# Kernel optimization log

Hardware: AMD Instinct MI355X
Metric: run time of the kernel (lower is better)

The kernel has to match this reference:

```python
import jax, jax.numpy as jnp
import numpy as np

N = 100000   # nodes
E = 1600000  # edges (avg degree 16)
H = 128      # hidden_channels
OUT = 64     # out_channels


def setup_inputs() -> dict:
    key = jax.random.key(0)
    ks = jax.random.split(key, 12)
    def lin(k, fan_in, fan_out):
        s = 1.0 / np.sqrt(fan_in)
        kw, kb = jax.random.split(k)
        W = jax.random.uniform(kw, (fan_in, fan_out), jnp.float32, -s, s)
        b = jax.random.uniform(kb, (fan_out,), jnp.float32, -s, s)
        return W, b
    W1, b1 = lin(ks[2], 1, H)
    W2, b2 = lin(ks[3], H, H)
    W3, b3 = lin(ks[4], H, H)
    Wo, bo = lin(ks[5], H, OUT)
    return {
        "x": jax.random.normal(ks[0], (N, 1), jnp.float32),
        "edge_index": jax.random.randint(ks[1], (2, E), 0, N, jnp.int32),
        "W1": W1, "b1": b1,
        "W2": W2, "b2": b2,
        "W3": W3, "b3": b3,
        "Wo": Wo, "bo": bo,
    }


def _gcn_conv(x, W, b, src, dst, dinv):
    # PyG GCNConv: x' = W x, then deg-normalized scatter-add over edges (+bias)
    h = x @ W                              # [N, C_out]
    norm = dinv[src] * dinv[dst]           # [E+N]
    msg = h[src] * norm[:, None]           # gather + scale  [E+N, C_out]
    out = jax.ops.segment_sum(msg, dst, num_segments=N)  # scatter-add
    return out + b


def reference(x, edge_index, W1, b1, W2, b2, W3, b3, Wo, bo):
    # add self-loops (GCNConv default add_self_loops=True)
    loop = jnp.arange(N, dtype=edge_index.dtype)
    src = jnp.concatenate([edge_index[0], loop])
    dst = jnp.concatenate([edge_index[1], loop])
    # symmetric normalization: deg over destination nodes, weight=1
    deg = jax.ops.segment_sum(jnp.ones_like(dst, jnp.float32), dst, num_segments=N)
    dinv = jnp.where(deg > 0, jax.lax.rsqrt(jnp.maximum(deg, 1.0)), 0.0)

    # layer 1: GCNConv -> dropout(eval=identity) -> relu
    h = jax.nn.relu(_gcn_conv(x, W1, b1, src, dst, dinv))
    # mid layer (num_layers=3 -> one mid block): GCNConv -> dropout -> relu
    h = jax.nn.relu(_gcn_conv(h, W2, b2, src, dst, dinv))
    # last layer: GCNConv -> dropout (no relu)
    h = _gcn_conv(h, W3, b3, src, dst, dinv)
    # linear head
    return h @ Wo + bo
```

## Files before the change

### kernel.cpp

```cpp
#include <hip/hip_runtime.h>

#define GN 100000
#define GE 1600000
#define GH 128
#define GOUT 64

#define NBUCK 391
#define BK 256
#define BCAP 4608
#define P1B 196
#define P1E 8192

#define NPW 5
#define CAPE 110
#define CAPW 112

typedef _Float16 half8v __attribute__((ext_vector_type(8)));
typedef _Float16 half4v __attribute__((ext_vector_type(4)));
typedef _Float16 half2v __attribute__((ext_vector_type(2)));
typedef float floatx4 __attribute__((ext_vector_type(4)));

__device__ __forceinline__ float dot2acc(half2v a, half2v b, float c) {
#if __has_builtin(__builtin_amdgcn_fdot2)
  return __builtin_amdgcn_fdot2(a, b, c, false);
#else
  return fmaf((float)a[0], (float)b[0], fmaf((float)a[1], (float)b[1], c));
#endif
}


__global__ __launch_bounds__(512) void k_zero(int* __restrict__ gCnt) {
  gCnt[threadIdx.x] = 0;
}


__global__ __launch_bounds__(1024) void p1_prep(const int* __restrict__ ei, int* __restrict__ gCnt,
                                                unsigned* __restrict__ staged,
                                                const float* __restrict__ W1, const float* __restrict__ b1,
                                                const float* __restrict__ W2, const float* __restrict__ W3,
                                                const float* __restrict__ Wo, const float* __restrict__ b3,
                                                const float* __restrict__ bo, unsigned* __restrict__ tabS,
                                                float* __restrict__ knots, _Float16* __restrict__ Wch,
                                                float* __restrict__ bch, int* __restrict__ rowStart) {
  int tid = threadIdx.x;
  int blk = blockIdx.x;
  if (blk < P1B) {
    __shared__ int cur[NBUCK];
    __shared__ int base[NBUCK];
    if (tid < NBUCK) cur[tid] = 0;
    __syncthreads();
    int e0 = blk * P1E;
    int sv[8], dv[8];
#pragma unroll
    for (int k = 0; k < 8; ++k) {
      int e = e0 + k * 1024 + tid;
      if (e < GE) {
        sv[k] = ei[e];
        dv[k] = ei[GE + e];
      } else {
        sv[k] = 0;
        dv[k] = -1;
      }
    }
#pragma unroll
    for (int k = 0; k < 8; ++k) {
      if (dv[k] >= 0) atomicAdd(&cur[dv[k] >> 8], 1);
    }
    __syncthreads();
    if (tid < NBUCK) {
      base[tid] = atomicAdd(&gCnt[tid], cur[tid]);
      cur[tid] = 0;
    }
    __syncthreads();
#pragma unroll
    for (int k = 0; k < 8; ++k) {
      if (dv[k] >= 0) {
        int bb = dv[k] >> 8;
        int r = atomicAdd(&cur[bb], 1);
        int pos = base[bb] + r;
        if (pos < BCAP) staged[(size_t)bb * BCAP + pos] = ((unsigned)sv[k] << 8) | (unsigned)(dv[k] & 255);
      }
    }
  } else if (blk == P1B) {
    __shared__ _Float16 sW2[GH * GH];
    __shared__ float sW1[GH], sb1[GH], th[GH];
    __shared__ int sidx[GH];
    for (int i = tid; i < GH * GH / 4; i += 1024) {
      float4 v = ((const float4*)W2)[i];
      half4v h;
      h[0] = (_Float16)v.x; h[1] = (_Float16)v.y; h[2] = (_Float16)v.z; h[3] = (_Float16)v.w;
      ((half4v*)sW2)[i] = h;
    }
    if (tid < GH) {
      float w1 = W1[tid], bb = b1[tid];
      sW1[tid] = w1;
      sb1[tid] = bb;
      th[tid] = (w1 != 0.0f) ? (-bb / w1) : 3.0e38f;
    }
    __syncthreads();
    if (tid < GH) {
      float my = th[tid];
      int r = 0;
      for (int j = 0; j < GH; ++j) {
        float tj = th[j];
        r += (tj < my) || (tj == my && j < tid);
      }
      sidx[r] = tid;
      knots[r] = my;
    }
    __syncthreads();
    if (tid < GH) {
      int c = tid;
      float A = 0.f, B = 0.f;
      for (int k = 0; k < GH; ++k) {
        float w1 = sW1[k];
        float w2 = (float)sW2[k * GH + c];
        if (w1 < 0.0f) {
          A = fmaf(w1, w2, A);
          B = fmaf(sb1[k], w2, B);
        } else if (w1 == 0.0f && sb1[k] > 0.0f) {
          B = fmaf(sb1[k], w2, B);
        }
      }
      for (int b = 0; b <= GH; ++b) {
        half2v hh;
        hh[0] = (_Float16)A;
        hh[1] = (_Float16)B;
        tabS[((b * 64 + (c >> 1)) << 1) + (c & 1)] = __builtin_bit_cast(unsigned, hh);
        if (b < GH) {
          int k = sidx[b];
          float w1 = sW1[k];
          float w2 = (float)sW2[k * GH + c];
          if (w1 > 0.0f) {
            A = fmaf(w1, w2, A);
            B = fmaf(sb1[k], w2, B);
          } else if (w1 < 0.0f) {
            A = fmaf(-w1, w2, A);
            B = fmaf(-sb1[k], w2, B);
          }
        }
      }
    }
  } else if (blk <= P1B + 8) {
    int idx = (blk - P1B - 1) * 1024 + tid;
    int k = idx >> 6, c = idx & 63;
    float s = 0.f;
#pragma unroll 8
    for (int j = 0; j < GH; ++j) s = fmaf(W3[k * GH + j], Wo[j * GOUT + c], s);
    Wch[idx] = (_Float16)s;
  } else {
    if (tid < GOUT) {
      float s = bo[tid];
      for (int j = 0; j < GH; ++j) s = fmaf(b3[j], Wo[j * GOUT + tid], s);
      bch[tid] = s;
    }
    if (tid == 1023) rowStart[GN] = GE;
  }
}


__global__ __launch_bounds__(1024) void p2a_build(const unsigned* __restrict__ staged,
                                                  const int* __restrict__ gCnt, const float* __restrict__ x,
                                                  float* __restrict__ dinv, float* __restrict__ xs,
                                                  int* __restrict__ rowStart) {
  __shared__ int cntL[BK];
  __shared__ int wsum[4];
  __shared__ int totL[NBUCK];
  __shared__ int baseSh;
  int b = blockIdx.x;
  int tid = threadIdx.x;
  if (tid < NBUCK) totL[tid] = gCnt[tid];
  if (tid < BK) cntL[tid] = 0;
  __syncthreads();
  if (tid == 0) {
    int s = 0;
    for (int j = 0; j < b; ++j) s += totL[j];
    baseSh = s;
  }
  int n = totL[b];
  if (n > BCAP) n = BCAP;
  __syncthreads();
  int base = baseSh;
  const unsigned* st = staged + (size_t)b * BCAP;
  for (int i = tid; i < n; i += 1024) atomicAdd(&cntL[st[i] & 255], 1);
  __syncthreads();
  int v = (tid < BK) ? cntL[tid] : 0;
  int lane = tid & 63, w = tid >> 6;
  int inc = v;
#pragma unroll
  for (int off = 1; off < 64; off <<= 1) {
    int u = __shfl_up(inc, off, 64);
    if (lane >= off) inc += u;
  }
  if (tid < BK && lane == 63) wsum[w] = inc;
  __syncthreads();
  if (tid < BK) {
    int woff = 0;
    for (int i = 0; i < w; ++i) woff += wsum[i];
    int ex = inc - v + woff;
    int node = b * BK + tid;
    if (node < GN) {
      rowStart[node] = base + ex;
      float dv = rsqrtf((float)(v + 1));
      dinv[node] = dv;
      xs[node] = x[node] * dv;
    }
  }
}


__global__ __launch_bounds__(1024) void p2b_scatter(const unsigned* __restrict__ staged,
                                                    const int* __restrict__ gCnt, const float* __restrict__ xs,
                                                    const float* __restrict__ dinv, const int* __restrict__ rowStart,
                                                    const float* __restrict__ knots, int* __restrict__ csr,
                                                    uint2* __restrict__ pqb) {
  __shared__ int curL[BK];
  __shared__ float accL[BK];
  __shared__ float kn[GH];
  int b = blockIdx.x;
  int tid = threadIdx.x;
  if (tid < GH) kn[tid] = knots[tid];
  int base = rowStart[b * BK];
  int node = b * BK + tid;
  if (tid < BK) {
    curL[tid] = (node < GN) ? (rowStart[node] - base) : 0;
    accL[tid] = 0.f;
  }
  int n = gCnt[b];
  if (n > BCAP) n = BCAP;
  __syncthreads();
  const unsigned* st = staged + (size_t)b * BCAP;
  int i = tid;
  for (; i + 3072 < n; i += 4096) {
    unsigned u0 = st[i], u1 = st[i + 1024], u2 = st[i + 2048], u3 = st[i + 3072];
    float x0 = xs[u0 >> 8], x1 = xs[u1 >> 8], x2 = xs[u2 >> 8], x3 = xs[u3 >> 8];
    int p0 = atomicAdd(&curL[u0 & 255], 1);
    csr[base + p0] = (int)(u0 >> 8);
    atomicAdd(&accL[u0 & 255], x0);
    int p1 = atomicAdd(&curL[u1 & 255], 1);
    csr[base + p1] = (int)(u1 >> 8);
    atomicAdd(&accL[u1 & 255], x1);
    int p2 = atomicAdd(&curL[u2 & 255], 1);
    csr[base + p2] = (int)(u2 >> 8);
    atomicAdd(&accL[u2 & 255], x2);
    int p3 = atomicAdd(&curL[u3 & 255], 1);
    csr[base + p3] = (int)(u3 >> 8);
    atomicAdd(&accL[u3 & 255], x3);
  }
  for (; i < n; i += 1024) {
    unsigned u = st[i];
    float xv = xs[u >> 8];
    int p = atomicAdd(&curL[u & 255], 1);
    csr[base + p] = (int)(u >> 8);
    atomicAdd(&accL[u & 255], xv);
  }
  __syncthreads();
  if (tid < BK && node < GN) {
    float q = dinv[node];
    float u = (accL[tid] + xs[node]) * q;
    int lo = 0;
#pragma unroll
    for (int s = 64; s > 0; s >>= 1)
      if (kn[lo + s - 1] < u) lo += s;
    if (lo < GH && kn[lo] < u) ++lo;
    half2v ph;
    ph[0] = (_Float16)(u * q);
    ph[1] = (_Float16)q;
    pqb[node] = make_uint2(__builtin_bit_cast(unsigned, ph), (unsigned)(lo << 9));
  }
}


__global__ __launch_bounds__(1024, 8) void k_exp_full(const uint2* __restrict__ pqb, const int* __restrict__ csr,
                                                      const int* __restrict__ rowStart, const unsigned* __restrict__ tabS,
                                                      const float* __restrict__ dinv, const float* __restrict__ b2,
                                                      _Float16* __restrict__ h2out) {
  __shared__ __align__(16) uint2 sTab[129 * 64];
  __shared__ __align__(16) uint2 sBuf[16 * CAPW];
  int tid = threadIdx.x;
  {
    const uint4* tg = (const uint4*)tabS;
    uint4* td = (uint4*)sTab;
    for (int i = tid; i < 4128; i += 1024) td[i] = tg[i];
  }
  int lane = tid & 63, wv = tid >> 6;
  int h = lane >> 5;
  int l = lane & 31;
  int wid = blockIdx.x * 16 + wv;
  int n0 = wid * NPW;
  int wl = lane <= NPW ? lane : NPW;
  int rsv = rowStart[n0 + wl];
  int eBeg = __builtin_amdgcn_readlane(rsv, 0);
  int eTot = __builtin_amdgcn_readlane(rsv, NPW) - eBeg;
  int nE = eTot < CAPE ? eTot : CAPE;
  int eClamp = eBeg < GE - 1 ? eBeg : GE - 1;
  int srcv[2];
#pragma unroll
  for (int c = 0; c < 2; ++c) {
    int i = c * 64 + lane;
    srcv[c] = csr[i < nE ? eBeg + i : eClamp];
  }
  uint2 pv[2];
#pragma unroll
  for (int c = 0; c < 2; ++c) pv[c] = pqb[srcv[c]];
  uint2* bw = sBuf + wv * CAPW;
#pragma unroll
  for (int c = 0; c < 2; ++c) {
    int i = c * 64 + lane;
    if (i < nE) bw[i] = pv[c];
  }
  __syncthreads();

  const char* tbl16 = (const char*)sTab + l * 16;
  const char* bwB = (const char*)bw;
  float4 bb4 = ((const float4*)b2)[l];

  float a0 = 0.f, a1 = 0.f, a2 = 0.f, a3 = 0.f;
  auto fdot4 = [&](uint4 t, unsigned pm) {
    half2v ph = __builtin_bit_cast(half2v, pm);
    a0 = dot2acc(__builtin_bit_cast(half2v, t.x), ph, a0);
    a1 = dot2acc(__builtin_bit_cast(half2v, t.y), ph, a1);
    a2 = dot2acc(__builtin_bit_cast(half2v, t.z), ph, a2);
    a3 = dot2acc(__builtin_bit_cast(half2v, t.w), ph, a3);
  };
  auto procM = [&](uint2 v) {
    unsigned pm = (h == 0) ? v.x : 0u;
    uint4 t = *(const uint4*)(tbl16 + v.y);
    fdot4(t, pm);
  };

  int sB = 0;
  for (int d = 0; d < NPW; ++d) {
    int sE = __builtin_amdgcn_readlane(rsv, d + 1) - eBeg;
    a0 = 0.f; a1 = 0.f; a2 = 0.f; a3 = 0.f;
    int lim = sE < nE ? sE : nE;
    int j = sB;
    for (; j + 8 <= lim; j += 8) {
      const char* p = bwB + (size_t)(j + h) * 8;
      uint2 v0 = *(const uint2*)(p);
      uint2 v1 = *(const uint2*)(p + 16);
      uint2 v2 = *(const uint2*)(p + 32);
      uint2 v3 = *(const uint2*)(p + 48);
      uint4 t0 = *(const uint4*)(tbl16 + v0.y);
      uint4 t1 = *(const uint4*)(tbl16 + v1.y);
      uint4 t2 = *(const uint4*)(tbl16 + v2.y);
      uint4 t3 = *(const uint4*)(tbl16 + v3.y);
      fdot4(t0, v0.x);
      fdot4(t1, v1.x);
      fdot4(t2, v2.x);
      fdot4(t3, v3.x);
    }
    for (; j + 2 <= lim; j += 2) {
      uint2 v = *(const uint2*)(bwB + (size_t)(j + h) * 8);
      uint4 t = *(const uint4*)(tbl16 + v.y);
      fdot4(t, v.x);
    }
    if (j < lim) procM(*(const uint2*)(bwB + (size_t)j * 8));
    for (int j2 = (sB > nE ? sB : nE); j2 < sE; ++j2) {
      int s2 = csr[eBeg + j2];
      procM(pqb[s2]);
    }
    procM(pqb[n0 + d]);
    a0 += __shfl_xor(a0, 32);
    a1 += __shfl_xor(a1, 32);
    a2 += __shfl_xor(a2, 32);
    a3 += __shfl_xor(a3, 32);
    if (h == 0) {
      float dvv = dinv[n0 + d];
      float r0 = fmaxf(fmaf(a0, dvv, bb4.x), 0.f);
      float r1 = fmaxf(fmaf(a1, dvv, bb4.y), 0.f);
      float r2 = fmaxf(fmaf(a2, dvv, bb4.z), 0.f);
      float r3 = fmaxf(fmaf(a3, dvv, bb4.w), 0.f);
      half2v o01, o23;
      o01[0] = (_Float16)r0; o01[1] = (_Float16)r1;
      o23[0] = (_Float16)r2; o23[1] = (_Float16)r3;
      uint2 ov;
      ov.x = __builtin_bit_cast(unsigned, o01);
      ov.y = __builtin_bit_cast(unsigned, o23);
      ((uint2*)h2out)[(size_t)(n0 + d) * 32 + l] = ov;
    }
    sB = sE;
  }
}


template <int NCOL>
__global__ __launch_bounds__(256) void gemm_f16k(const _Float16* __restrict__ A, const _Float16* __restrict__ Wh,
                                                 const float* __restrict__ dinv, _Float16* __restrict__ Cout,
                                                 int ntiles) {
  constexpr int NT = NCOL / 16;
  constexpr int WS = 136;
  __shared__ __align__(16) _Float16 WtL[NCOL * WS];
  int tid = threadIdx.x;
  for (int i = tid; i < GH * NCOL; i += 256) {
    int k = i / NCOL, n = i % NCOL;
    WtL[n * WS + k] = Wh[i];
  }
  __syncthreads();
  int lane = tid & 63;
  int waveId = tid >> 6;
  int m = lane & 15, q = lane >> 4;

  for (int t = blockIdx.x * 4 + waveId; t < ntiles; t += gridDim.x * 4) {
    int row = t * 16 + m;
    const _Float16* arow = A + (size_t)row * GH + q * 8;
    half8v af[4];
#pragma unroll
    for (int ks = 0; ks < 4; ++ks) af[ks] = *(const half8v*)(arow + ks * 32);
    floatx4 acc[NT];
#pragma unroll
    for (int nt = 0; nt < NT; ++nt) {
      floatx4 z = {0.0f, 0.0f, 0.0f, 0.0f};
      acc[nt] = z;
    }
#pragma unroll
    for (int ks = 0; ks < 4; ++ks) {
#pragma unroll
      for (int nt = 0; nt < NT; ++nt) {
        half8v wf = *(const half8v*)(&WtL[(nt * 16 + m) * WS + ks * 32 + q * 8]);
        acc[nt] = __builtin_amdgcn_mfma_f32_16x16x32_f16(wf, af[ks], acc[nt], 0, 0, 0);
      }
    }
    float sc = dinv[row];
    _Float16* crow = Cout + (size_t)row * NCOL;
#pragma unroll
    for (int nt = 0; nt < NT; ++nt) {
      half4v h;
#pragma unroll
      for (int j = 0; j < 4; ++j) h[j] = (_Float16)(acc[nt][j] * sc);
      *(half4v*)(crow + nt * 16 + q * 4) = h;
    }
  }
}


__global__ __launch_bounds__(256) void k_agg64(const _Float16* __restrict__ ht, const int* __restrict__ rowStart,
                                               const int* __restrict__ csr, const float* __restrict__ dinv,
                                               const float* __restrict__ bias, float* __restrict__ out) {
  int tid = threadIdx.x;
  int lane = tid & 63;
  int wave = (blockIdx.x << 2) + (tid >> 6);
  int g = lane >> 4;
  int l = lane & 15;
  int d = (wave << 2) + g;
  const uint2* h2p = (const uint2*)ht;
  float ax = 0.f, ay = 0.f, az = 0.f, aw = 0.f;
  auto acc4 = [&](uint2 r) {
    half2v lo = __builtin_bit_cast(half2v, r.x);
    half2v hi = __builtin_bit_cast(half2v, r.y);
    ax += (float)lo[0];
    ay += (float)lo[1];
    az += (float)hi[0];
    aw += (float)hi[1];
  };
  acc4(h2p[(size_t)d * 16 + l]);
  int e = rowStart[d];
  int en = rowStart[d + 1];
  uint2 rA0, rA1, rA2, rA3, rB0, rB1, rB2, rB3;
  bool hA = (e + 4 <= en);
  if (hA) {
    int s0 = csr[e], s1 = csr[e + 1], s2 = csr[e + 2], s3 = csr[e + 3];
    rA0 = h2p[(size_t)s0 * 16 + l]; rA1 = h2p[(size_t)s1 * 16 + l];
    rA2 = h2p[(size_t)s2 * 16 + l]; rA3 = h2p[(size_t)s3 * 16 + l];
  }
  bool hB = (e + 8 <= en);
  if (hB) {
    int s0 = csr[e + 4], s1 = csr[e + 5], s2 = csr[e + 6], s3 = csr[e + 7];
    rB0 = h2p[(size_t)s0 * 16 + l]; rB1 = h2p[(size_t)s1 * 16 + l];
    rB2 = h2p[(size_t)s2 * 16 + l]; rB3 = h2p[(size_t)s3 * 16 + l];
  }
  while (hA) {
    bool hC = (e + 12 <= en);
    uint2 rC0, rC1, rC2, rC3;
    if (hC) {
      int n0 = csr[e + 8], n1 = csr[e + 9], n2 = csr[e + 10], n3 = csr[e + 11];
      rC0 = h2p[(size_t)n0 * 16 + l]; rC1 = h2p[(size_t)n1 * 16 + l];
      rC2 = h2p[(size_t)n2 * 16 + l]; rC3 = h2p[(size_t)n3 * 16 + l];
    }
    acc4(rA0); acc4(rA1); acc4(rA2); acc4(rA3);
    rA0 = rB0; rA1 = rB1; rA2 = rB2; rA3 = rB3;
    rB0 = rC0; rB1 = rC1; rB2 = rC2; rB3 = rC3;
    e += 4;
    hA = hB;
    hB = hC;
  }
  for (; e < en; ++e) acc4(h2p[(size_t)csr[e] * 16 + l]);
  float dv = dinv[d];
  float4 bb = ((const float4*)bias)[l];
  float4 o;
  o.x = fmaf(ax, dv, bb.x);
  o.y = fmaf(ay, dv, bb.y);
  o.z = fmaf(az, dv, bb.z);
  o.w = fmaf(aw, dv, bb.w);
  ((float4*)out)[(size_t)d * 16 + l] = o;
}


extern "C" void kernel_launch(void* const* d_in, const int* in_sizes, int n_in,
                              void* d_out, int out_size, void* d_ws, size_t ws_size,
                              hipStream_t stream) {
  const float* x  = (const float*)d_in[0];
  const int*   ei = (const int*)d_in[1];
  const float* W1 = (const float*)d_in[2];
  const float* b1 = (const float*)d_in[3];
  const float* W2 = (const float*)d_in[4];
  const float* b2 = (const float*)d_in[5];
  const float* W3 = (const float*)d_in[6];
  const float* b3 = (const float*)d_in[7];
  const float* Wo = (const float*)d_in[8];
  const float* bo = (const float*)d_in[9];
  float* out = (float*)d_out;

  char* ws = (char*)d_ws;
  size_t off = 0;
  auto alloc = [&](size_t bytes) -> char* {
    off = (off + 255) & ~(size_t)255;
    char* p = ws + off;
    off += bytes;
    return p;
  };
  float*     dinv      = (float*)alloc((size_t)GN * 4);
  float*     xs        = (float*)alloc((size_t)GN * 4);
  int*       rowStart  = (int*)alloc((size_t)(GN + 1) * 4);
  int*       gCnt      = (int*)alloc((size_t)512 * 4);
  int*       csr       = (int*)alloc((size_t)GE * 4);
  unsigned*  tabS      = (unsigned*)alloc((size_t)129 * 128 * 4);
  float*     knots     = (float*)alloc((size_t)GH * 4);
  _Float16*  Wch       = (_Float16*)alloc((size_t)GH * GOUT * 2);
  float*     bch       = (float*)alloc((size_t)GOUT * 4);
  uint2*     pqb       = (uint2*)alloc((size_t)GN * 8);
  _Float16*  bufA      = (_Float16*)alloc((size_t)GN * GH * 2);
  _Float16*  bufB      = (_Float16*)alloc((size_t)GN * GOUT * 2);
  unsigned*  staged    = (unsigned*)bufA;
  (void)ws_size; (void)in_sizes; (void)n_in; (void)out_size;

  const int NTILES = GN / 16;
  const int GEMM_GRID = 782;

  k_zero<<<1, 512, 0, stream>>>(gCnt);
  p1_prep<<<P1B + 10, 1024, 0, stream>>>(ei, gCnt, staged, W1, b1, W2, W3, Wo, b3, bo,
                                         tabS, knots, Wch, bch, rowStart);

  p2a_build<<<NBUCK, 1024, 0, stream>>>(staged, gCnt, x, dinv, xs, rowStart);
  p2b_scatter<<<NBUCK, 1024, 0, stream>>>(staged, gCnt, xs, dinv, rowStart, knots, csr, pqb);

  k_exp_full<<<1250, 1024, 0, stream>>>(pqb, csr, rowStart, tabS, dinv, b2, bufA);

  gemm_f16k<GOUT><<<GEMM_GRID, 256, 0, stream>>>(bufA, Wch, dinv, bufB, NTILES);
  k_agg64<<<6250, 256, 0, stream>>>(bufB, rowStart, csr, dinv, bch, out);
}
```

Before: 222.6 us.

## Fuse output-projection GEMM into the layer-2 aggregation kernel

The separate gemm_f16k launch is removed and its MFMA projection is appended to k_exp_full. Each block first aggregates its 80 nodes, then reuses the table shared memory to hold the transposed Wch. Five of its waves then multiply the freshly written h2 rows by Wch and write the scaled fp16 result for k_agg64. This drops one kernel launch and lets the h2 rows be re-read while they are likely still in cache rather than in a separate pass. In exchange, 11 of 16 waves sit idle during the GEMM tail, and the block relies on __syncthreads for visibility of its own global writes.

```diff
diff --git a/kernel.cpp b/kernel.cpp
--- a/kernel.cpp
+++ b/kernel.cpp
@@ -274,7 +274,8 @@
 __global__ __launch_bounds__(1024, 8) void k_exp_full(const uint2* __restrict__ pqb, const int* __restrict__ csr,
                                                       const int* __restrict__ rowStart, const unsigned* __restrict__ tabS,
                                                       const float* __restrict__ dinv, const float* __restrict__ b2,
-                                                      _Float16* __restrict__ h2out) {
+                                                      const _Float16* __restrict__ Wch, _Float16* __restrict__ h2out,
+                                                      _Float16* __restrict__ t3out) {
   __shared__ __align__(16) uint2 sTab[129 * 64];
   __shared__ __align__(16) uint2 sBuf[16 * CAPW];
   int tid = threadIdx.x;
@@ -311,124 +312,116 @@
   }
   __syncthreads();
 
-  const char* tbl16 = (const char*)sTab + l * 16;
-  const char* bwB = (const char*)bw;
-  float4 bb4 = ((const float4*)b2)[l];
-
-  float a0 = 0.f, a1 = 0.f, a2 = 0.f, a3 = 0.f;
-  auto fdot4 = [&](uint4 t, unsigned pm) {
-    half2v ph = __builtin_bit_cast(half2v, pm);
-    a0 = dot2acc(__builtin_bit_cast(half2v, t.x), ph, a0);
-    a1 = dot2acc(__builtin_bit_cast(half2v, t.y), ph, a1);
-    a2 = dot2acc(__builtin_bit_cast(half2v, t.z), ph, a2);
-    a3 = dot2acc(__builtin_bit_cast(half2v, t.w), ph, a3);
-  };
-  auto procM = [&](uint2 v) {
-    unsigned pm = (h == 0) ? v.x : 0u;
-    uint4 t = *(const uint4*)(tbl16 + v.y);
-    fdot4(t, pm);
-  };
-
-  int sB = 0;
-  for (int d = 0; d < NPW; ++d) {
-    int sE = __builtin_amdgcn_readlane(rsv, d + 1) - eBeg;
-    a0 = 0.f; a1 = 0.f; a2 = 0.f; a3 = 0.f;
-    int lim = sE < nE ? sE : nE;
-    int j = sB;
-    for (; j + 8 <= lim; j += 8) {
-      const char* p = bwB + (size_t)(j + h) * 8;
-      uint2 v0 = *(const uint2*)(p);
-      uint2 v1 = *(const uint2*)(p + 16);
-      uint2 v2 = *(const uint2*)(p + 32);
-      uint2 v3 = *(const uint2*)(p + 48);
-      uint4 t0 = *(const uint4*)(tbl16 + v0.y);
-      uint4 t1 = *(const uint4*)(tbl16 + v1.y);
-      uint4 t2 = *(const uint4*)(tbl16 + v2.y);
-      uint4 t3 = *(const uint4*)(tbl16 + v3.y);
-      fdot4(t0, v0.x);
-      fdot4(t1, v1.x);
-      fdot4(t2, v2.x);
-      fdot4(t3, v3.x);
-    }
-    for (; j + 2 <= lim; j += 2) {
-      uint2 v = *(const uint2*)(bwB + (size_t)(j + h) * 8);
+  {
+    const char* tbl16 = (const char*)sTab + l * 16;
+    const char* bwB = (const char*)bw;
+    float4 bb4 = ((const float4*)b2)[l];
+
+    float a0 = 0.f, a1 = 0.f, a2 = 0.f, a3 = 0.f;
+    auto fdot4 = [&](uint4 t, unsigned pm) {
+      half2v ph = __builtin_bit_cast(half2v, pm);
+      a0 = dot2acc(__builtin_bit_cast(half2v, t.x), ph, a0);
+      a1 = dot2acc(__builtin_bit_cast(half2v, t.y), ph, a1);
+      a2 = dot2acc(__builtin_bit_cast(half2v, t.z), ph, a2);
+      a3 = dot2acc(__builtin_bit_cast(half2v, t.w), ph, a3);
+    };
+    auto procM = [&](uint2 v) {
+      unsigned pm = (h == 0) ? v.x : 0u;
       uint4 t = *(const uint4*)(tbl16 + v.y);
-      fdot4(t, v.x);
-    }
-    if (j < lim) procM(*(const uint2*)(bwB + (size_t)j * 8));
-    for (int j2 = (sB > nE ? sB : nE); j2 < sE; ++j2) {
-      int s2 = csr[eBeg + j2];
-      procM(pqb[s2]);
-    }
-    procM(pqb[n0 + d]);
-    a0 += __shfl_xor(a0, 32);
-    a1 += __shfl_xor(a1, 32);
-    a2 += __shfl_xor(a2, 32);
-    a3 += __shfl_xor(a3, 32);
-    if (h == 0) {
-      float dvv = dinv[n0 + d];
-      float r0 = fmaxf(fmaf(a0, dvv, bb4.x), 0.f);
-      float r1 = fmaxf(fmaf(a1, dvv, bb4.y), 0.f);
-      float r2 = fmaxf(fmaf(a2, dvv, bb4.z), 0.f);
-      float r3 = fmaxf(fmaf(a3, dvv, bb4.w), 0.f);
-      half2v o01, o23;
-      o01[0] = (_Float16)r0; o01[1] = (_Float16)r1;
-      o23[0] = (_Float16)r2; o23[1] = (_Float16)r3;
-      uint2 ov;
-      ov.x = __builtin_bit_cast(unsigned, o01);
-      ov.y = __builtin_bit_cast(unsigned, o23);
-      ((uint2*)h2out)[(size_t)(n0 + d) * 32 + l] = ov;
-    }
-    sB = sE;
-  }
-}
-
-
-template <int NCOL>
-__global__ __launch_bounds__(256) void gemm_f16k(const _Float16* __restrict__ A, const _Float16* __restrict__ Wh,
-                                                 const float* __restrict__ dinv, _Float16* __restrict__ Cout,
-                                                 int ntiles) {
-  constexpr int NT = NCOL / 16;
+      fdot4(t, pm);
+    };
+
+    int sB = 0;
+    for (int d = 0; d < NPW; ++d) {
+      int sE = __builtin_amdgcn_readlane(rsv, d + 1) - eBeg;
+      a0 = 0.f; a1 = 0.f; a2 = 0.f; a3 = 0.f;
+      int lim = sE < nE ? sE : nE;
+      int j = sB;
+      for (; j + 8 <= lim; j += 8) {
+        const char* p = bwB + (size_t)(j + h) * 8;
+        uint2 v0 = *(const uint2*)(p);
+        uint2 v1 = *(const uint2*)(p + 16);
+        uint2 v2 = *(const uint2*)(p + 32);
+        uint2 v3 = *(const uint2*)(p + 48);
+        uint4 t0 = *(const uint4*)(tbl16 + v0.y);
+        uint4 t1 = *(const uint4*)(tbl16 + v1.y);
+        uint4 t2 = *(const uint4*)(tbl16 + v2.y);
+        uint4 t3 = *(const uint4*)(tbl16 + v3.y);
+        fdot4(t0, v0.x);
+        fdot4(t1, v1.x);
+        fdot4(t2, v2.x);
+        fdot4(t3, v3.x);
+      }
+      for (; j + 2 <= lim; j += 2) {
+        uint2 v = *(const uint2*)(bwB + (size_t)(j + h) * 8);
+        uint4 t = *(const uint4*)(tbl16 + v.y);
+        fdot4(t, v.x);
+      }
+      if (j < lim) procM(*(const uint2*)(bwB + (size_t)j * 8));
+      for (int j2 = (sB > nE ? sB : nE); j2 < sE; ++j2) {
+        int s2 = csr[eBeg + j2];
+        procM(pqb[s2]);
+      }
+      procM(pqb[n0 + d]);
+      a0 += __shfl_xor(a0, 32);
+      a1 += __shfl_xor(a1, 32);
+      a2 += __shfl_xor(a2, 32);
+      a3 += __shfl_xor(a3, 32);
+      if (h == 0) {
+        float dvv = dinv[n0 + d];
+        float r0 = fmaxf(fmaf(a0, dvv, bb4.x), 0.f);
+        float r1 = fmaxf(fmaf(a1, dvv, bb4.y), 0.f);
+        float r2 = fmaxf(fmaf(a2, dvv, bb4.z), 0.f);
+        float r3 = fmaxf(fmaf(a3, dvv, bb4.w), 0.f);
+        half2v o01, o23;
+        o01[0] = (_Float16)r0; o01[1] = (_Float16)r1;
+        o23[0] = (_Float16)r2; o23[1] = (_Float16)r3;
+        uint2 ov;
+        ov.x = __builtin_bit_cast(unsigned, o01);
+        ov.y = __builtin_bit_cast(unsigned, o23);
+        ((uint2*)h2out)[(size_t)(n0 + d) * 32 + l] = ov;
+      }
+      sB = sE;
+    }
+  }
+
   constexpr int WS = 136;
-  __shared__ __align__(16) _Float16 WtL[NCOL * WS];
-  int tid = threadIdx.x;
-  for (int i = tid; i < GH * NCOL; i += 256) {
-    int k = i / NCOL, n = i % NCOL;
-    WtL[n * WS + k] = Wh[i];
-  }
-  __syncthreads();
-  int lane = tid & 63;
-  int waveId = tid >> 6;
-  int m = lane & 15, q = lane >> 4;
-
-  for (int t = blockIdx.x * 4 + waveId; t < ntiles; t += gridDim.x * 4) {
-    int row = t * 16 + m;
-    const _Float16* arow = A + (size_t)row * GH + q * 8;
+  _Float16* WtL = (_Float16*)sTab;
+  __syncthreads();
+  for (int i = tid; i < GH * GOUT; i += 1024) {
+    int k = i >> 6, n = i & 63;
+    WtL[n * WS + k] = Wch[i];
+  }
+  __syncthreads();
+  if (wv < 5) {
+    int m = lane & 15, q = lane >> 4;
+    int row = blockIdx.x * 80 + wv * 16 + m;
+    const _Float16* arow = h2out + (size_t)row * GH + q * 8;
     half8v af[4];
 #pragma unroll
     for (int ks = 0; ks < 4; ++ks) af[ks] = *(const half8v*)(arow + ks * 32);
-    floatx4 acc[NT];
-#pragma unroll
-    for (int nt = 0; nt < NT; ++nt) {
+    floatx4 acc[4];
+#pragma unroll
+    for (int nt = 0; nt < 4; ++nt) {
       floatx4 z = {0.0f, 0.0f, 0.0f, 0.0f};
       acc[nt] = z;
     }
 #pragma unroll
     for (int ks = 0; ks < 4; ++ks) {
 #pragma unroll
-      for (int nt = 0; nt < NT; ++nt) {
+      for (int nt = 0; nt < 4; ++nt) {
         half8v wf = *(const half8v*)(&WtL[(nt * 16 + m) * WS + ks * 32 + q * 8]);
         acc[nt] = __builtin_amdgcn_mfma_f32_16x16x32_f16(wf, af[ks], acc[nt], 0, 0, 0);
       }
     }
     float sc = dinv[row];
-    _Float16* crow = Cout + (size_t)row * NCOL;
-#pragma unroll
-    for (int nt = 0; nt < NT; ++nt) {
-      half4v h;
-#pragma unroll
-      for (int j = 0; j < 4; ++j) h[j] = (_Float16)(acc[nt][j] * sc);
-      *(half4v*)(crow + nt * 16 + q * 4) = h;
+    _Float16* crow = t3out + (size_t)row * GOUT;
+#pragma unroll
+    for (int nt = 0; nt < 4; ++nt) {
+      half4v hv;
+#pragma unroll
+      for (int j = 0; j < 4; ++j) hv[j] = (_Float16)(acc[nt][j] * sc);
+      *(half4v*)(crow + nt * 16 + q * 4) = hv;
     }
   }
 }
@@ -534,9 +527,6 @@
   unsigned*  staged    = (unsigned*)bufA;
   (void)ws_size; (void)in_sizes; (void)n_in; (void)out_size;
 
-  const int NTILES = GN / 16;
-  const int GEMM_GRID = 782;
-
   k_zero<<<1, 512, 0, stream>>>(gCnt);
   p1_prep<<<P1B + 10, 1024, 0, stream>>>(ei, gCnt, staged, W1, b1, W2, W3, Wo, b3, bo,
                                          tabS, knots, Wch, bch, rowStart);
@@ -544,8 +534,7 @@
   p2a_build<<<NBUCK, 1024, 0, stream>>>(staged, gCnt, x, dinv, xs, rowStart);
   p2b_scatter<<<NBUCK, 1024, 0, stream>>>(staged, gCnt, xs, dinv, rowStart, knots, csr, pqb);
 
-  k_exp_full<<<1250, 1024, 0, stream>>>(pqb, csr, rowStart, tabS, dinv, b2, bufA);
-
-  gemm_f16k<GOUT><<<GEMM_GRID, 256, 0, stream>>>(bufA, Wch, dinv, bufB, NTILES);
+  k_exp_full<<<1250, 1024, 0, stream>>>(pqb, csr, rowStart, tabS, dinv, b2, Wch, bufA, bufB);
+
   k_agg64<<<6250, 256, 0, stream>>>(bufB, rowStart, csr, dinv, bch, out);
 }
```

Measured after the change: 217.6 us (median of 2 runs). 1.02x faster.
